# Performance work log

Measured on AMD Instinct MI355X. Metric: run time of the kernel, lower is better.

Reference implementation:

```python
import jax, jax.numpy as jnp
import numpy as np

D = 64          # embed_dim == latent dim
T = 200         # diffusion_steps, timestep_respacing='' -> full 200 reverse steps
B, L = 8192, 100
N_ITEMS = 100000


def setup_inputs() -> dict:
    key = jax.random.key(0)
    ks = jax.random.split(key, 16)

    def lin(k, i, o):
        return (jax.random.normal(k, (i, o), jnp.float32) / np.sqrt(i)).astype(jnp.float32)

    item_seq = jax.random.randint(ks[0], (B, L), 0, N_ITEMS)
    item_emb = jax.random.normal(ks[1], (N_ITEMS, D), jnp.float32) * 0.02
    item_emb = item_emb.at[0].set(0.0)  # padding_idx=0
    return {
        'item_seq': item_seq,
        'item_emb': item_emb,
        'W_enc1': lin(ks[2], D, 256), 'b_enc1': jnp.zeros((256,), jnp.float32),
        'W_enc2': lin(ks[3], 256, 2 * D), 'b_enc2': jnp.zeros((2 * D,), jnp.float32),
        'W_in': lin(ks[4], D, D), 'b_in': jnp.zeros((D,), jnp.float32),
        'W_t': lin(ks[5], D, D), 'b_t': jnp.zeros((D,), jnp.float32),
        'W_c': lin(ks[6], D, D), 'b_c': jnp.zeros((D,), jnp.float32),
        'W_out': lin(ks[7], D, D), 'b_out': jnp.zeros((D,), jnp.float32),
    }


def _schedule():
    # improved-diffusion linear schedule
    scale = 1000.0 / T
    betas = jnp.linspace(scale * 1e-4, scale * 0.02, T, dtype=jnp.float32)
    alphas = 1.0 - betas
    acp = jnp.cumprod(alphas)
    acp_prev = jnp.concatenate([jnp.ones((1,), jnp.float32), acp[:-1]])
    sqrt_recip = jnp.sqrt(1.0 / acp)
    sqrt_recipm1 = jnp.sqrt(1.0 / acp - 1.0)
    post_var = betas * (1.0 - acp_prev) / (1.0 - acp)
    post_logvar = jnp.log(jnp.concatenate([post_var[1:2], post_var[1:]]))  # clipped
    coef1 = betas * jnp.sqrt(acp_prev) / (1.0 - acp)
    coef2 = (1.0 - acp_prev) * jnp.sqrt(alphas) / (1.0 - acp)
    return sqrt_recip, sqrt_recipm1, post_logvar, coef1, coef2


def reference(item_seq, item_emb, W_enc1, b_enc1, W_enc2, b_enc2,
              W_in, b_in, W_t, b_t, W_c, b_c, W_out, b_out):
    # ---- pooled VAE encoder (eval mode: dropout = identity, z = mu) ----
    seq = item_emb[item_seq]                                   # [B, L, D] gather
    cnt = jnp.sum(item_seq != 0, axis=1, keepdims=True).astype(seq.dtype)
    pooled = jnp.sum(seq, axis=1) / jnp.sqrt(cnt)              # [B, D]
    h = jax.nn.relu(pooled @ W_enc1 + b_enc1)
    enc = h @ W_enc2 + b_enc2                                  # [B, 2D]
    mu, logvar = jnp.split(enc, 2, axis=-1)
    z = mu                                                     # eval reparameterize

    # ---- ScoreNet: eps-prediction MLP conditioned on x_start and sinusoidal t ----
    half = D // 2
    freqs = jnp.exp(-jnp.log(10000.0) * jnp.arange(half, dtype=jnp.float32) / half)

    def scorenet(x, t_float, cond):
        ang = t_float * freqs                                  # [D/2]
        temb = jnp.concatenate([jnp.cos(ang), jnp.sin(ang)])   # [D]
        hh = jax.nn.silu(x @ W_in + b_in + (temb @ W_t + b_t) + cond @ W_c + b_c)
        return hh @ W_out + b_out                              # eps, [B, D]

    # ---- p_sample_loop (FIXED_SMALL variance, clip_denoised=True) ----
    sqrt_recip, sqrt_recipm1, post_logvar, coef1, coef2 = _schedule()
    x_init = jax.random.normal(jax.random.key(1), z.shape, z.dtype)
    noise_key = jax.random.key(2)

    def step(x, t):
        eps = scorenet(x, t.astype(jnp.float32), z)
        x0 = jnp.clip(sqrt_recip[t] * x - sqrt_recipm1[t] * eps, -1.0, 1.0)
        mean = coef1[t] * x0 + coef2[t] * x
        noise = jax.random.normal(jax.random.fold_in(noise_key, t), x.shape, x.dtype)
        sigma = jnp.where(t > 0, jnp.exp(0.5 * post_logvar[t]), 0.0)
        return mean + sigma * noise, None

    sample, _ = jax.lax.scan(step, x_init, jnp.arange(T - 1, -1, -1))
    return sample
```

## Files before the change

kernel.cpp:

```cpp
#include <hip/hip_runtime.h>
#include <cstdint>


#define DEVI __device__ __forceinline__

typedef __attribute__((ext_vector_type(8))) short short8;
typedef __attribute__((ext_vector_type(4))) float f32x4;

DEVI void threefry2x32(uint32_t k0, uint32_t k1, uint32_t x0, uint32_t x1,
                       uint32_t &o0, uint32_t &o1)
{
  const uint32_t ks2 = k0 ^ k1 ^ 0x1BD11BDAu;
  x0 += k0; x1 += k1;
#define TFR(r) { x0 += x1; x1 = __builtin_rotateleft32(x1, r); x1 ^= x0; }
  TFR(13u) TFR(15u) TFR(26u) TFR(6u)   x0 += k1;  x1 += ks2 + 1u;
  TFR(17u) TFR(29u) TFR(16u) TFR(24u)  x0 += ks2; x1 += k0 + 2u;
  TFR(13u) TFR(15u) TFR(26u) TFR(6u)   x0 += k0;  x1 += k1 + 3u;
  TFR(17u) TFR(29u) TFR(16u) TFR(24u)  x0 += k1;  x1 += ks2 + 4u;
  TFR(13u) TFR(15u) TFR(26u) TFR(6u)   x0 += ks2; x1 += k0 + 5u;
#undef TFR
  o0 = x0; o1 = x1;
}

DEVI uint32_t jax_random_bits32(uint32_t k0, uint32_t k1, uint32_t j)
{
  uint32_t a, b;
  threefry2x32(k0, k1, 0u, j, a, b);
  return a ^ b;
}

DEVI float jax_bits_to_normal(uint32_t bits)
{
  const float LO = -0.99999994f;
  float f = __uint_as_float((bits >> 9) | 0x3f800000u) - 1.0f;
  float u = fmaxf(LO, f * 2.0f + LO);
  float w = -__logf((1.0f - u) * (1.0f + u));
  float p;
  if (w < 5.0f) {
    w = w - 2.5f;
    p =              2.81022636e-08f;
    p = fmaf(p, w,   3.43273939e-07f);
    p = fmaf(p, w,  -3.5233877e-06f);
    p = fmaf(p, w,  -4.39150654e-06f);
    p = fmaf(p, w,   0.00021858087f);
    p = fmaf(p, w,  -0.00125372503f);
    p = fmaf(p, w,  -0.00417768164f);
    p = fmaf(p, w,   0.246640727f);
    p = fmaf(p, w,   1.50140941f);
  } else {
    w = sqrtf(w) - 3.0f;
    p =             -0.000200214257f;
    p = fmaf(p, w,   0.000100950558f);
    p = fmaf(p, w,   0.00134934322f);
    p = fmaf(p, w,  -0.00367342844f);
    p = fmaf(p, w,   0.00573950773f);
    p = fmaf(p, w,  -0.0076224613f);
    p = fmaf(p, w,   0.00943887047f);
    p = fmaf(p, w,   1.00167406f);
    p = fmaf(p, w,   2.83297682f);
  }
  return 1.41421356237f * (p * u);
}

DEVI short bf16_hi_trunc(float x) { return (short)(__float_as_uint(x) >> 16); }
DEVI float bf16_to_f32(short h)
{
  return __uint_as_float(((uint32_t)(unsigned short)h) << 16);
}
DEVI void split_bf16(float x, short &h, short &l)
{
  h = bf16_hi_trunc(x);
  float r = x - bf16_to_f32(h);
  l = bf16_hi_trunc(r);
}

DEVI short8 ld_frag16(const short* p)
{
  union { int4 v; short8 s; } u;
  u.v = *(const int4*)p;
  return u.s;
}

__global__ __launch_bounds__(256)
void k_pool(const int* __restrict__ seq, const float* __restrict__ emb,
            float* __restrict__ pooled)
{
  const int lane = threadIdx.x & 63;
  const int r    = blockIdx.x * 4 + (threadIdx.x >> 6);
  const int* row = seq + r * 100;
  float s = 0.f;
  int cnt = 0;
  for (int l = 0; l < 100; ++l) {
    int id = row[l];
    cnt += (id != 0);
    s += emb[id * 64 + lane];
  }
  pooled[r * 64 + lane] = s / sqrtf((float)cnt);
}

__global__ __launch_bounds__(256)
void k_enc(const float* __restrict__ pooled,
           const float* __restrict__ W1, const float* __restrict__ b1,
           const float* __restrict__ W2, const float* __restrict__ b2,
           const float* __restrict__ Wc, const float* __restrict__ bc,
           float* __restrict__ cproj)
{
  __shared__ float p_s[8][64];
  __shared__ float h_s[8][256];
  __shared__ float mu_s[8][64];
  const int tid = threadIdx.x;
  const int r0  = blockIdx.x * 8;

  for (int i = tid; i < 8 * 64; i += 256)
    p_s[i >> 6][i & 63] = pooled[r0 * 64 + i];
  __syncthreads();

  float hacc[8];
#pragma unroll
  for (int r = 0; r < 8; ++r) hacc[r] = b1[tid];
  for (int k = 0; k < 64; ++k) {
    float w = W1[k * 256 + tid];
#pragma unroll
    for (int r = 0; r < 8; ++r) hacc[r] = fmaf(p_s[r][k], w, hacc[r]);
  }
#pragma unroll
  for (int r = 0; r < 8; ++r) h_s[r][tid] = fmaxf(hacc[r], 0.f);
  __syncthreads();

#pragma unroll
  for (int pass = 0; pass < 2; ++pass) {
    int r = pass * 4 + (tid >> 6);
    int j = tid & 63;
    float acc = b2[j];
    for (int k = 0; k < 256; ++k)
      acc = fmaf(h_s[r][k], W2[k * 128 + j], acc);
    mu_s[r][j] = acc;
  }
  __syncthreads();

#pragma unroll
  for (int pass = 0; pass < 2; ++pass) {
    int r = pass * 4 + (tid >> 6);
    int j = tid & 63;
    float acc = bc[j];
    for (int k = 0; k < 64; ++k)
      acc = fmaf(mu_s[r][k], Wc[k * 64 + j], acc);
    cproj[(r0 + r) * 64 + j] = acc;
  }
}

__global__ __launch_bounds__(64)
void k_prep(const float* __restrict__ Wt, const float* __restrict__ bt,
            const float* __restrict__ bin, float* __restrict__ tpb,
            float* __restrict__ sched)
{
  __shared__ float temb[64];
  const int t = blockIdx.x;
  const int d = threadIdx.x;
  const float lg = logf(10000.0f);
  {
    int i = d & 31;
    float fr  = expf((-lg * (float)i) / 32.0f);
    float ang = (float)t * fr;
    temb[d] = (d < 32) ? cosf(ang) : sinf(ang);
  }
  if (d == 0) {
    const float start = (float)(5.0 * 1e-4);
    const float stop  = (float)(5.0 * 0.02);
    const float delta = stop - start;
    float prod = 1.f, acp_prev = 1.f, beta = 0.f, alpha = 1.f;
    for (int i = 0; i <= t; ++i) {
      beta  = start + ((float)i * delta) / 199.0f;
      alpha = 1.0f - beta;
      acp_prev = prod;
      prod = prod * alpha;
    }
    float acp = prod;
    float om  = 1.0f - acp;
    sched[t * 8 + 0] = sqrtf(1.0f / acp);
    sched[t * 8 + 1] = sqrtf(1.0f / acp - 1.0f);
    sched[t * 8 + 2] = beta * sqrtf(acp_prev) / om;
    sched[t * 8 + 3] = (1.0f - acp_prev) * sqrtf(alpha) / om;
    float pv = beta * (1.0f - acp_prev) / om;
    sched[t * 8 + 4] = (t > 0) ? sqrtf(pv) : 0.0f;
    uint32_t fk0, fk1;
    threefry2x32(0u, 2u, 0u, (uint32_t)t, fk0, fk1);
    ((uint32_t*)sched)[t * 8 + 5] = fk0;
    ((uint32_t*)sched)[t * 8 + 6] = fk1;
  }
  __syncthreads();
  float acc = bt[d] + bin[d];
  for (int k = 0; k < 64; ++k)
    acc = fmaf(temb[k], Wt[k * 64 + d], acc);
  tpb[t * 64 + d] = acc;
}

#define XLDW  72
#define NBW   68

__global__
__attribute__((amdgpu_flat_work_group_size(512, 512), amdgpu_waves_per_eu(4, 4)))
void k_ddpm(const float* __restrict__ Win, const float* __restrict__ Wout,
            const float* __restrict__ bout,
            const float* __restrict__ cproj, const float* __restrict__ tpb,
            const float* __restrict__ sched, float* __restrict__ out)
{
  __shared__ __align__(16) short Xh[16 * XLDW], Xl[16 * XLDW];
  __shared__ __align__(16) short Hh[16 * XLDW], Hl[16 * XLDW];
  __shared__ __align__(16) float nbuf[2 * 16 * NBW];

  const int tid  = threadIdx.x;
  const int lane = tid & 63;
  const int w    = tid >> 6;
  const bool gemv = (w < 4);
  const int r0g  = blockIdx.x * 16;
  const uint32_t* su = (const uint32_t*)sched;

  const int nt   = w & 3;
  const int nn   = lane & 15;
  const int quad = lane >> 4;
  const int dim  = nt * 16 + nn;
  const int arow = nn;
  const int kq0  = quad * 8;
  const int kq1  = 32 + quad * 8;
  const int rowb = quad * 4;

  const int cb   = w * 128 + lane * 2;
  const uint32_t jn = (uint32_t)(r0g * 64 + cb);
  const int nrow = cb >> 6;
  const int ndim = cb & 63;
  float* nb_w = &nbuf[nrow * NBW + ndim];

  short8 wiH0, wiL0, wiH1, wiL1, woH0, woL0, woH1, woL1;
  float cp[4] = {0.f, 0.f, 0.f, 0.f}, xo[4] = {0.f, 0.f, 0.f, 0.f};
  float bo = 0.f, tp = 0.f;
  uint32_t j0 = 0;

  if (gemv) {
#pragma unroll
    for (int j = 0; j < 8; ++j) {
      short h, l;
      split_bf16(Win[(kq0 + j) * 64 + dim], h, l);  wiH0[j] = h; wiL0[j] = l;
      split_bf16(Win[(kq1 + j) * 64 + dim], h, l);  wiH1[j] = h; wiL1[j] = l;
      split_bf16(Wout[(kq0 + j) * 64 + dim], h, l); woH0[j] = h; woL0[j] = l;
      split_bf16(Wout[(kq1 + j) * 64 + dim], h, l); woH1[j] = h; woL1[j] = l;
    }
    bo = bout[dim];
    j0 = (uint32_t)((r0g + rowb) * 64 + dim);
#pragma unroll
    for (int r = 0; r < 4; ++r) cp[r] = cproj[j0 + r * 64u];
#pragma unroll
    for (int r = 0; r < 4; ++r) {
      xo[r] = jax_bits_to_normal(jax_random_bits32(0u, 1u, j0 + r * 64u));
      short h, l;
      split_bf16(xo[r], h, l);
      Xh[(rowb + r) * XLDW + dim] = h; Xl[(rowb + r) * XLDW + dim] = l;
    }
    tp = tpb[199 * 64 + dim];
  }
  {
    const uint32_t fk0 = su[199 * 8 + 5];
    const uint32_t fk1 = su[199 * 8 + 6];
    float* d = nb_w + 16 * NBW;
    d[0] = jax_bits_to_normal(jax_random_bits32(fk0, fk1, jn + 0u));
    d[1] = jax_bits_to_normal(jax_random_bits32(fk0, fk1, jn + 1u));
  }
  __syncthreads();

#pragma unroll 1
  for (int t = 199; t >= 0; --t) {
    uint32_t gk0 = 0, gk1 = 0;
    float* nd = nullptr;
    if (t > 0) {
      gk0 = su[(t - 1) * 8 + 5];
      gk1 = su[(t - 1) * 8 + 6];
      nd = nb_w + ((t - 1) & 1) * 16 * NBW;
    }

    float sr = 0.f, srm1 = 0.f, c1 = 0.f, c2 = 0.f, sg = 0.f, tpn = 0.f;
    f32x4 acc;

    if (gemv) {
      sr   = sched[t * 8 + 0];
      srm1 = sched[t * 8 + 1];
      c1   = sched[t * 8 + 2];
      c2   = sched[t * 8 + 3];
      sg   = sched[t * 8 + 4];

#pragma unroll
      for (int r = 0; r < 4; ++r) acc[r] = tp + cp[r];
      {
        short8 xh0 = ld_frag16(&Xh[arow * XLDW + kq0]);
        short8 xl0 = ld_frag16(&Xl[arow * XLDW + kq0]);
        short8 xh1 = ld_frag16(&Xh[arow * XLDW + kq1]);
        short8 xl1 = ld_frag16(&Xl[arow * XLDW + kq1]);
        acc = __builtin_amdgcn_mfma_f32_16x16x32_bf16(xl0, wiH0, acc, 0, 0, 0);
        acc = __builtin_amdgcn_mfma_f32_16x16x32_bf16(xh0, wiL0, acc, 0, 0, 0);
        acc = __builtin_amdgcn_mfma_f32_16x16x32_bf16(xh0, wiH0, acc, 0, 0, 0);
        acc = __builtin_amdgcn_mfma_f32_16x16x32_bf16(xl1, wiH1, acc, 0, 0, 0);
        acc = __builtin_amdgcn_mfma_f32_16x16x32_bf16(xh1, wiL1, acc, 0, 0, 0);
        acc = __builtin_amdgcn_mfma_f32_16x16x32_bf16(xh1, wiH1, acc, 0, 0, 0);
      }
#pragma unroll
      for (int r = 0; r < 4; ++r) {
        float v = acc[r];
        v = v * __builtin_amdgcn_rcpf(1.0f + __expf(-v));
        short h, l;
        split_bf16(v, h, l);
        Hh[(rowb + r) * XLDW + dim] = h; Hl[(rowb + r) * XLDW + dim] = l;
      }
      int tn = (t > 0) ? (t - 1) : 0;
      tpn = tpb[tn * 64 + dim];
    }
    if (t > 0)
      nd[0] = jax_bits_to_normal(jax_random_bits32(gk0, gk1, jn + 0u));
    __syncthreads();

    if (gemv) {
      float n[4];
      const float* nr = &nbuf[(t & 1) * 16 * NBW + rowb * NBW + dim];
#pragma unroll
      for (int r = 0; r < 4; ++r) n[r] = nr[r * NBW];

      f32x4 eac;
#pragma unroll
      for (int r = 0; r < 4; ++r) eac[r] = bo;
      {
        short8 hh0 = ld_frag16(&Hh[arow * XLDW + kq0]);
        short8 hl0 = ld_frag16(&Hl[arow * XLDW + kq0]);
        short8 hh1 = ld_frag16(&Hh[arow * XLDW + kq1]);
        short8 hl1 = ld_frag16(&Hl[arow * XLDW + kq1]);
        eac = __builtin_amdgcn_mfma_f32_16x16x32_bf16(hl0, woH0, eac, 0, 0, 0);
        eac = __builtin_amdgcn_mfma_f32_16x16x32_bf16(hh0, woL0, eac, 0, 0, 0);
        eac = __builtin_amdgcn_mfma_f32_16x16x32_bf16(hh0, woH0, eac, 0, 0, 0);
        eac = __builtin_amdgcn_mfma_f32_16x16x32_bf16(hl1, woH1, eac, 0, 0, 0);
        eac = __builtin_amdgcn_mfma_f32_16x16x32_bf16(hh1, woL1, eac, 0, 0, 0);
        eac = __builtin_amdgcn_mfma_f32_16x16x32_bf16(hh1, woH1, eac, 0, 0, 0);
      }
#pragma unroll
      for (int r = 0; r < 4; ++r) {
        float xc = fminf(1.f, fmaxf(-1.f, sr * xo[r] - srm1 * eac[r]));
        xo[r] = c1 * xc + c2 * xo[r] + sg * n[r];
        short h, l;
        split_bf16(xo[r], h, l);
        Xh[(rowb + r) * XLDW + dim] = h; Xl[(rowb + r) * XLDW + dim] = l;
      }
      tp = tpn;
    }
    if (t > 0)
      nd[1] = jax_bits_to_normal(jax_random_bits32(gk0, gk1, jn + 1u));
    __syncthreads();
  }

  if (gemv) {
#pragma unroll
    for (int r = 0; r < 4; ++r) out[j0 + r * 64u] = xo[r];
  }
}

extern "C" void kernel_launch(void* const* d_in, const int* in_sizes, int n_in,
                              void* d_out, int out_size, void* d_ws, size_t ws_size,
                              hipStream_t stream)
{
  const int*   seq  = (const int*)  d_in[0];
  const float* emb  = (const float*)d_in[1];
  const float* W1   = (const float*)d_in[2];
  const float* b1   = (const float*)d_in[3];
  const float* W2   = (const float*)d_in[4];
  const float* b2   = (const float*)d_in[5];
  const float* Win  = (const float*)d_in[6];
  const float* bin  = (const float*)d_in[7];
  const float* Wt   = (const float*)d_in[8];
  const float* bt   = (const float*)d_in[9];
  const float* Wc   = (const float*)d_in[10];
  const float* bc   = (const float*)d_in[11];
  const float* Wout = (const float*)d_in[12];
  const float* bout = (const float*)d_in[13];

  float* out   = (float*)d_out;
  float* ws    = (float*)d_ws;
  float* cproj = ws;
  float* tpb   = ws + 524288;
  float* sched = ws + 524288 + 12800;
  float* pooled = out;

  k_pool <<<2048, 256, 0, stream>>>(seq, emb, pooled);
  k_enc  <<<1024, 256, 0, stream>>>(pooled, W1, b1, W2, b2, Wc, bc, cproj);
  k_prep <<<200, 64, 0, stream>>>(Wt, bt, bin, tpb, sched);
  k_ddpm <<<512, 512, 0, stream>>>(Win, Wout, bout, cproj, tpb, sched, out);
}
```

Before: 530.3 us.

## Fuse pooling and encoder into DDPM kernel; batch noise RNG bit generation

Removes the separate pooling and encoder kernels and computes the pooled embedding, the MLP encoder and the condition projection inside the DDPM kernel for each block's 16 rows, keeping intermediates in a shared-memory buffer that is later reused for the DDPM tiles. This drops two launches and the global round trip for pooled and cproj. It also computes both threefry noise bit words before the first barrier and converts them to normals after the second. The tradeoff is that the encoder prologue now runs on only 512 blocks with scalar FMAs, and the 100-id gather per row is done by fewer threads, so the prologue may serialize work that used to be spread across many more blocks.

```diff
diff --git a/kernel.cpp b/kernel.cpp
--- a/kernel.cpp
+++ b/kernel.cpp
@@ -81,74 +81,6 @@
   return u.s;
 }
 
-__global__ __launch_bounds__(256)
-void k_pool(const int* __restrict__ seq, const float* __restrict__ emb,
-            float* __restrict__ pooled)
-{
-  const int lane = threadIdx.x & 63;
-  const int r    = blockIdx.x * 4 + (threadIdx.x >> 6);
-  const int* row = seq + r * 100;
-  float s = 0.f;
-  int cnt = 0;
-  for (int l = 0; l < 100; ++l) {
-    int id = row[l];
-    cnt += (id != 0);
-    s += emb[id * 64 + lane];
-  }
-  pooled[r * 64 + lane] = s / sqrtf((float)cnt);
-}
-
-__global__ __launch_bounds__(256)
-void k_enc(const float* __restrict__ pooled,
-           const float* __restrict__ W1, const float* __restrict__ b1,
-           const float* __restrict__ W2, const float* __restrict__ b2,
-           const float* __restrict__ Wc, const float* __restrict__ bc,
-           float* __restrict__ cproj)
-{
-  __shared__ float p_s[8][64];
-  __shared__ float h_s[8][256];
-  __shared__ float mu_s[8][64];
-  const int tid = threadIdx.x;
-  const int r0  = blockIdx.x * 8;
-
-  for (int i = tid; i < 8 * 64; i += 256)
-    p_s[i >> 6][i & 63] = pooled[r0 * 64 + i];
-  __syncthreads();
-
-  float hacc[8];
-#pragma unroll
-  for (int r = 0; r < 8; ++r) hacc[r] = b1[tid];
-  for (int k = 0; k < 64; ++k) {
-    float w = W1[k * 256 + tid];
-#pragma unroll
-    for (int r = 0; r < 8; ++r) hacc[r] = fmaf(p_s[r][k], w, hacc[r]);
-  }
-#pragma unroll
-  for (int r = 0; r < 8; ++r) h_s[r][tid] = fmaxf(hacc[r], 0.f);
-  __syncthreads();
-
-#pragma unroll
-  for (int pass = 0; pass < 2; ++pass) {
-    int r = pass * 4 + (tid >> 6);
-    int j = tid & 63;
-    float acc = b2[j];
-    for (int k = 0; k < 256; ++k)
-      acc = fmaf(h_s[r][k], W2[k * 128 + j], acc);
-    mu_s[r][j] = acc;
-  }
-  __syncthreads();
-
-#pragma unroll
-  for (int pass = 0; pass < 2; ++pass) {
-    int r = pass * 4 + (tid >> 6);
-    int j = tid & 63;
-    float acc = bc[j];
-    for (int k = 0; k < 64; ++k)
-      acc = fmaf(mu_s[r][k], Wc[k * 64 + j], acc);
-    cproj[(r0 + r) * 64 + j] = acc;
-  }
-}
-
 __global__ __launch_bounds__(64)
 void k_prep(const float* __restrict__ Wt, const float* __restrict__ bt,
             const float* __restrict__ bin, float* __restrict__ tpb,
@@ -200,14 +132,16 @@
 
 __global__
 __attribute__((amdgpu_flat_work_group_size(512, 512), amdgpu_waves_per_eu(4, 4)))
-void k_ddpm(const float* __restrict__ Win, const float* __restrict__ Wout,
+void k_ddpm(const int* __restrict__ seq, const float* __restrict__ emb,
+            const float* __restrict__ W1, const float* __restrict__ b1,
+            const float* __restrict__ W2, const float* __restrict__ b2,
+            const float* __restrict__ Wc, const float* __restrict__ bc,
+            const float* __restrict__ Win, const float* __restrict__ Wout,
             const float* __restrict__ bout,
-            const float* __restrict__ cproj, const float* __restrict__ tpb,
-            const float* __restrict__ sched, float* __restrict__ out)
-{
-  __shared__ __align__(16) short Xh[16 * XLDW], Xl[16 * XLDW];
-  __shared__ __align__(16) short Hh[16 * XLDW], Hl[16 * XLDW];
-  __shared__ __align__(16) float nbuf[2 * 16 * NBW];
+            const float* __restrict__ tpb, const float* __restrict__ sched,
+            float* __restrict__ out)
+{
+  __shared__ __align__(16) char smem[28672];
 
   const int tid  = threadIdx.x;
   const int lane = tid & 63;
@@ -229,10 +163,79 @@
   const uint32_t jn = (uint32_t)(r0g * 64 + cb);
   const int nrow = cb >> 6;
   const int ndim = cb & 63;
+
+  {
+    float* pool_s = (float*)smem;
+    float* h_s    = (float*)(smem + 4096);
+    float* mu_s   = (float*)(smem + 20480);
+    float* cp_s   = (float*)(smem + 24576);
+
+#pragma unroll
+    for (int i = 0; i < 2; ++i) {
+      int c = tid + i * 512;
+      int row = c >> 6, d = c & 63;
+      const int* rowp = seq + (r0g + row) * 100;
+      float s = 0.f; int cnt = 0;
+      for (int l = 0; l < 100; ++l) {
+        int id = rowp[l];
+        cnt += (id != 0);
+        s += emb[id * 64 + d];
+      }
+      pool_s[row * 64 + d] = s / sqrtf((float)cnt);
+    }
+    __syncthreads();
+
+#pragma unroll
+    for (int i = 0; i < 8; ++i) {
+      int c = tid + i * 512;
+      int row = c >> 8, j = c & 255;
+      float a = b1[j];
+      for (int k = 0; k < 64; ++k)
+        a = fmaf(pool_s[row * 64 + k], W1[k * 256 + j], a);
+      h_s[row * 256 + j] = fmaxf(a, 0.f);
+    }
+    __syncthreads();
+
+#pragma unroll
+    for (int i = 0; i < 2; ++i) {
+      int c = tid + i * 512;
+      int row = c >> 6, j = c & 63;
+      float a = b2[j];
+      for (int k = 0; k < 256; ++k)
+        a = fmaf(h_s[row * 256 + k], W2[k * 128 + j], a);
+      mu_s[row * 64 + j] = a;
+    }
+    __syncthreads();
+
+#pragma unroll
+    for (int i = 0; i < 2; ++i) {
+      int c = tid + i * 512;
+      int row = c >> 6, j = c & 63;
+      float a = bc[j];
+      for (int k = 0; k < 64; ++k)
+        a = fmaf(mu_s[row * 64 + k], Wc[k * 64 + j], a);
+      cp_s[row * 64 + j] = a;
+    }
+    __syncthreads();
+  }
+
+  float cp[4] = {0.f, 0.f, 0.f, 0.f};
+  if (gemv) {
+    const float* cp_s = (const float*)(smem + 24576);
+#pragma unroll
+    for (int r = 0; r < 4; ++r) cp[r] = cp_s[(rowb + r) * 64 + dim];
+  }
+  __syncthreads();
+
+  short* Xh = (short*)smem;
+  short* Xl = (short*)(smem + 2304);
+  short* Hh = (short*)(smem + 4608);
+  short* Hl = (short*)(smem + 6912);
+  float* nbuf = (float*)(smem + 9216);
   float* nb_w = &nbuf[nrow * NBW + ndim];
 
   short8 wiH0, wiL0, wiH1, wiL1, woH0, woL0, woH1, woL1;
-  float cp[4] = {0.f, 0.f, 0.f, 0.f}, xo[4] = {0.f, 0.f, 0.f, 0.f};
+  float xo[4] = {0.f, 0.f, 0.f, 0.f};
   float bo = 0.f, tp = 0.f;
   uint32_t j0 = 0;
 
@@ -247,8 +250,6 @@
     }
     bo = bout[dim];
     j0 = (uint32_t)((r0g + rowb) * 64 + dim);
-#pragma unroll
-    for (int r = 0; r < 4; ++r) cp[r] = cproj[j0 + r * 64u];
 #pragma unroll
     for (int r = 0; r < 4; ++r) {
       xo[r] = jax_bits_to_normal(jax_random_bits32(0u, 1u, j0 + r * 64u));
@@ -312,8 +313,11 @@
       int tn = (t > 0) ? (t - 1) : 0;
       tpn = tpb[tn * 64 + dim];
     }
-    if (t > 0)
-      nd[0] = jax_bits_to_normal(jax_random_bits32(gk0, gk1, jn + 0u));
+    uint32_t b0 = 0, b1v = 0;
+    if (t > 0) {
+      b0  = jax_random_bits32(gk0, gk1, jn + 0u);
+      b1v = jax_random_bits32(gk0, gk1, jn + 1u);
+    }
     __syncthreads();
 
     if (gemv) {
@@ -347,8 +351,10 @@
       }
       tp = tpn;
     }
-    if (t > 0)
-      nd[1] = jax_bits_to_normal(jax_random_bits32(gk0, gk1, jn + 1u));
+    if (t > 0) {
+      nd[0] = jax_bits_to_normal(b0);
+      nd[1] = jax_bits_to_normal(b1v);
+    }
     __syncthreads();
   }
 
@@ -379,13 +385,10 @@
 
   float* out   = (float*)d_out;
   float* ws    = (float*)d_ws;
-  float* cproj = ws;
-  float* tpb   = ws + 524288;
-  float* sched = ws + 524288 + 12800;
-  float* pooled = out;
-
-  k_pool <<<2048, 256, 0, stream>>>(seq, emb, pooled);
-  k_enc  <<<1024, 256, 0, stream>>>(pooled, W1, b1, W2, b2, Wc, bc, cproj);
+  float* tpb   = ws;
+  float* sched = ws + 12800;
+
   k_prep <<<200, 64, 0, stream>>>(Wt, bt, bin, tpb, sched);
-  k_ddpm <<<512, 512, 0, stream>>>(Win, Wout, bout, cproj, tpb, sched, out);
-}
+  k_ddpm <<<512, 512, 0, stream>>>(seq, emb, W1, b1, W2, b2, Wc, bc,
+                                   Win, Wout, bout, tpb, sched, out);
+}
```

Result: slower. 560.8 us (+5.8%).
